# Performance work log

Measured on AMD Instinct MI355X. Metric: run time of the kernel, lower is better.

Reference implementation:

```python
import jax, jax.numpy as jnp
import numpy as np

B, N, D, F, L, R = 16, 1024, 256, 128, 2, 2


def setup_inputs() -> dict:
    key = jax.random.key(0)
    ks = jax.random.split(key, 12)
    s = 0.05
    return {
        "node_embed": jax.random.normal(ks[0], (B, N, D), jnp.float32),
        "input_x": jax.random.normal(ks[1], (B, F), jnp.float32),
        "adj": jax.random.randint(ks[2], (R, B, N, N), 0, 2, jnp.int32),
        "WQi_w": jax.random.normal(ks[3], (L, F, F), jnp.float32) * s,
        "WQi_b": jnp.zeros((L, F), jnp.float32),
        "WQ_w": jax.random.normal(ks[4], (L, D + F, D), jnp.float32) * s,
        "WQ_b": jnp.zeros((L, D), jnp.float32),
        "WK_w": jax.random.normal(ks[5], (L, R, D + F, D), jnp.float32) * s,
        "WK_b": jnp.zeros((L, R, D), jnp.float32),
        "WV_w": jax.random.normal(ks[6], (L, R, D + F, D), jnp.float32) * s,
        "WV_b": jnp.zeros((L, R, D), jnp.float32),
        "WF_w": jax.random.normal(ks[7], (L, R * D, D), jnp.float32) * s,
        "WF_b": jnp.zeros((L, D), jnp.float32),
        "ln_g": jnp.ones((L, D), jnp.float32),
        "ln_b": jnp.zeros((L, D), jnp.float32),
    }


def _layer_norm(x, g, b, eps=1e-5):
    mu = jnp.mean(x, axis=-1, keepdims=True)
    var = jnp.var(x, axis=-1, keepdims=True)
    return (x - mu) * jax.lax.rsqrt(var + eps) * g + b


def reference(node_embed, input_x, adj, WQi_w, WQi_b, WQ_w, WQ_b,
              WK_w, WK_b, WV_w, WV_b, WF_w, WF_b, ln_g, ln_b):
    scale = 1.0 / (D ** 0.5)
    h = node_embed
    for l in range(L):
        # input feature projection, broadcast over nodes
        x1 = input_x @ WQi_w[l] + WQi_b[l]              # (B, F)
        x1 = jnp.broadcast_to(x1[:, None, :], (h.shape[0], h.shape[1], F))
        qc = jnp.concatenate([h, x1], axis=-1)          # (B, N, D+F)
        q = qc @ WQ_w[l] + WQ_b[l]                      # (B, N, D)
        outs = []
        for r in range(R):
            k = qc @ WK_w[l, r] + WK_b[l, r]            # (B, N, D)
            v = qc @ WV_w[l, r] + WV_b[l, r]            # (B, N, D)
            scores = jnp.einsum('bnd,bmd->bnm', q, k) * scale
            scores = jnp.where(adj[r] == 0, -1e9, scores)
            alpha = jax.nn.softmax(scores, axis=-1)
            outs.append(jnp.einsum('bnm,bmd->bnd', alpha, v))
        h_concat = jnp.concatenate(outs, axis=-1)       # (B, N, R*D)
        h_fused = jax.nn.relu(h_concat @ WF_w[l] + WF_b[l])
        h = _layer_norm(h + h_fused, ln_g[l], ln_b[l])
    return h
```

## Files before the change

kernel.cpp:

```cpp
#include <hip/hip_runtime.h>
#include <hip/hip_bf16.h>

#define BB 16
#define NN 1024
#define DD 256
#define FF_ 128
#define LL 2
#define RR 2
#define DF 384
#define MM (BB*NN)
#define NPROJ 1280
#define PK 768

typedef __attribute__((ext_vector_type(8))) short s16x8;
typedef __attribute__((ext_vector_type(4))) float f32x4;
typedef __attribute__((ext_vector_type(16))) float f32x16;
typedef __attribute__((ext_vector_type(2))) unsigned int u32x2;
typedef __attribute__((ext_vector_type(4))) unsigned int u32x4;
typedef __attribute__((ext_vector_type(4))) unsigned short us16x4;

__device__ __forceinline__ unsigned short f2bf(float f){
  unsigned u = __builtin_bit_cast(unsigned, f);
  u += 0x7fff + ((u >> 16) & 1);
  return (unsigned short)(u >> 16);
}

__device__ __forceinline__ void gload16(const void* g, void* l){
  __builtin_amdgcn_global_load_lds(
      (const __attribute__((address_space(1))) unsigned int*)g,
      (__attribute__((address_space(3))) unsigned int*)l, 16, 0, 0);
}

#define MFMA16(a,b,c) __builtin_amdgcn_mfma_f32_16x16x32_bf16((a),(b),(c),0,0,0)
#define MFMA32(a,b,c) __builtin_amdgcn_mfma_f32_32x32x16_bf16((a),(b),(c),0,0,0)

__global__ __launch_bounds__(256) void pack_adj(const int* __restrict__ adj,
                                                unsigned long long* __restrict__ bits){
  int w = threadIdx.x >> 6, lane = threadIdx.x & 63;
  size_t row = (size_t)blockIdx.x * 4 + w;
  const int* a = adj + row * NN;
  unsigned long long* brow = bits + row * 16;
  #pragma unroll
  for (int j = 0; j < 16; ++j){
    unsigned long long m = __ballot(a[j*64 + lane] != 0);
    if (lane == 0) brow[j] = m;
  }
}

#define PREP_WT   3840
#define PREP_WTF  1024
#define PREP_BALL 10
#define PREP_X1   16
#define PREP_H    2048
#define PREP_TOT  (PREP_WT+PREP_WTF+PREP_BALL+PREP_X1+PREP_H)

__global__ __launch_bounds__(256) void prep(
    const float* __restrict__ node, const float* __restrict__ inx,
    const float* __restrict__ WQi_w, const float* __restrict__ WQi_b,
    const float* __restrict__ WQ_w, const float* __restrict__ WK_w,
    const float* __restrict__ WV_w, const float* __restrict__ WQ_b,
    const float* __restrict__ WK_b, const float* __restrict__ WV_b,
    const float* __restrict__ WF_w,
    unsigned short* __restrict__ wtall, unsigned short* __restrict__ wtf,
    float* __restrict__ ball, unsigned short* __restrict__ x1bf,
    unsigned short* __restrict__ hbf){
  int bid = blockIdx.x, t = threadIdx.x;
  if (bid < PREP_WT){
    int o = bid*256 + t;
    int l = o / (NPROJ*DF); int oo = o - l*(NPROJ*DF);
    int n = oo / DF, k = oo - n*DF;
    const float* WQ = WQ_w + (size_t)l*DF*256;
    const float* WK = WK_w + (size_t)l*RR*DF*256;
    const float* WV = WV_w + (size_t)l*RR*DF*256;
    float v;
    if (n < 256)      v = WQ[(size_t)k*256 + n];
    else if (n < 768) v = WK[(size_t)((n-256)>>8)*(DF*256) + (size_t)k*256 + ((n-256)&255)];
    else              v = WV[(size_t)((n-768)>>8)*(DF*256) + (size_t)k*256 + ((n-768)&255)];
    wtall[o] = f2bf(v);
  } else if (bid < PREP_WT + PREP_WTF){
    int o = (bid - PREP_WT)*256 + t;
    int l = o >> 17; int oo = o & 131071;
    int n = oo >> 9, k = oo & 511;
    wtf[o] = f2bf(WF_w[(size_t)l*512*256 + (size_t)k*256 + n]);
  } else if (bid < PREP_WT + PREP_WTF + PREP_BALL){
    int o = (bid - PREP_WT - PREP_WTF)*256 + t;
    if (o < 2*NPROJ){
      int l = o / NPROJ, n = o - l*NPROJ;
      float v = (n < 256) ? WQ_b[l*256 + n]
              : (n < 768) ? WK_b[(size_t)l*512 + (n-256)]
                          : WV_b[(size_t)l*512 + (n-768)];
      ball[o] = v;
    }
  } else if (bid < PREP_WT + PREP_WTF + PREP_BALL + PREP_X1){
    int o = (bid - PREP_WT - PREP_WTF - PREP_BALL)*256 + t;
    int l = o >> 11, bj = o & 2047;
    int b = bj >> 7, j = bj & 127;
    const float* w = WQi_w + (size_t)l*FF_*FF_;
    float s = WQi_b[l*FF_ + j];
    for (int i = 0; i < FF_; ++i) s += inx[b*FF_ + i] * w[i*FF_ + j];
    x1bf[o] = f2bf(s);
  } else {
    int o = (bid - (PREP_TOT - PREP_H))*256 + t;
    const float4* src = (const float4*)node + (size_t)o*2;
    float4 a = src[0], c = src[1];
    uint4 pk;
    pk.x = (unsigned)f2bf(a.x) | ((unsigned)f2bf(a.y) << 16);
    pk.y = (unsigned)f2bf(a.z) | ((unsigned)f2bf(a.w) << 16);
    pk.z = (unsigned)f2bf(c.x) | ((unsigned)f2bf(c.y) << 16);
    pk.w = (unsigned)f2bf(c.z) | ((unsigned)f2bf(c.w) << 16);
    *(uint4*)(hbf + (size_t)o*8) = pk;
  }
}

__global__ __launch_bounds__(256) void gemm_big(const unsigned short* __restrict__ hbf,
    const unsigned short* __restrict__ x1l, const unsigned short* __restrict__ Wt,
    const float* __restrict__ bias, unsigned short* __restrict__ POUT,
    unsigned short* __restrict__ vtall){
  __shared__ unsigned short As[2][128*32];
  __shared__ unsigned short Bs[2][128*32];
  int t = threadIdx.x, lane = t & 63, w = t >> 6;
  int wr = w >> 1, wc = w & 1, l15 = lane & 15, lhi = lane >> 4;
  int bm = blockIdx.x, bn = blockIdx.y, bb = bm >> 3;
  f32x4 acc[4][4];
  #pragma unroll
  for (int m = 0; m < 4; ++m)
    #pragma unroll
    for (int n = 0; n < 4; ++n) acc[m][n] = (f32x4){0.f,0.f,0.f,0.f};

  auto STAGE = [&](int bi, int kk){
    #pragma unroll
    for (int i = 0; i < 2; ++i){
      int base = w*2048 + i*1024;
      int off = base + lane*16;
      int row = off >> 6, cb = off & 63;
      const char* asrc = (kk < 8)
        ? (const char*)hbf + ((size_t)(bm*128 + row)*256 + kk*32)*2 + cb
        : (const char*)x1l + ((size_t)bb*128 + (kk-8)*32)*2 + cb;
      gload16(asrc, (char*)As[bi] + base);
      gload16((const char*)Wt + ((size_t)(bn*128 + row)*DF + kk*32)*2 + cb,
              (char*)Bs[bi] + base);
    }
  };

  STAGE(0, 0);
  __syncthreads();
  for (int kk = 0; kk < 12; ++kk){
    int cur = kk & 1;
    if (kk + 1 < 12) STAGE(cur ^ 1, kk + 1);
    s16x8 af[4], bfr[4];
    #pragma unroll
    for (int m = 0; m < 4; ++m) af[m]  = *(const s16x8*)&As[cur][(wr*64 + m*16 + l15)*32 + lhi*8];
    #pragma unroll
    for (int n = 0; n < 4; ++n) bfr[n] = *(const s16x8*)&Bs[cur][(wc*64 + n*16 + l15)*32 + lhi*8];
    __builtin_amdgcn_s_setprio(1);
    #pragma unroll
    for (int m = 0; m < 4; ++m)
      #pragma unroll
      for (int n = 0; n < 4; ++n)
        acc[m][n] = MFMA16(af[m], bfr[n], acc[m][n]);
    __builtin_amdgcn_s_setprio(0);
    __syncthreads();
  }

  if (bn < 6){
    #pragma unroll
    for (int n = 0; n < 4; ++n){
      int gn = bn*128 + wc*64 + n*16 + l15;
      float bv = bias[gn];
      #pragma unroll
      for (int m = 0; m < 4; ++m){
        int gm = bm*128 + wr*64 + m*16 + lhi*4;
        #pragma unroll
        for (int i = 0; i < 4; ++i)
          POUT[(size_t)(gm + i)*PK + gn] = f2bf(acc[m][n][i] + bv);
      }
    }
  } else {
    #pragma unroll
    for (int n = 0; n < 4; ++n){
      int gn = bn*128 + wc*64 + n*16 + l15;
      float bv = bias[gn];
      int rv = gn - 768;
      int r = rv >> 8, d = rv & 255;
      #pragma unroll
      for (int m = 0; m < 4; ++m){
        int mb = (bm & 7)*128 + wr*64 + m*16 + lhi*4;
        us16x4 pk;
        #pragma unroll
        for (int i = 0; i < 4; ++i) pk[i] = f2bf(acc[m][n][i] + bv);
        *(us16x4*)(vtall + ((size_t)((r*16 + bb)*256 + d))*NN + mb) = pk;
      }
    }
  }
}

__global__ __launch_bounds__(512, 2) void attn6(const unsigned short* __restrict__ P,
    const unsigned short* __restrict__ VT, const unsigned long long* __restrict__ bits,
    unsigned short* __restrict__ hc){
  __shared__ char smem[135168];

  int t = threadIdx.x, lane = t & 63, w = t >> 6;
  int h = lane >> 5, l31 = lane & 31;
  int hh = w >> 2, qs = w & 3;
  int F = blockIdx.x;
  int xcd = F & 7, j = F >> 3;
  int qt = j & 7;
  int gidx = xcd*4 + (j >> 3);
  int b = gidx & 15, r = gidx >> 4;
  const float C = 0.09016844f;

  size_t kcol = 256 + (size_t)r*256;
  const unsigned short* Vb = VT + ((size_t)(r*16 + b))*256*NN;

  int qrow = qt*128 + qs*32 + l31;

  s16x8 qf[16];
  {
    const unsigned short* qp = P + ((size_t)(b*NN + qrow))*PK + h*8;
    #pragma unroll
    for (int d_ = 0; d_ < 16; ++d_) qf[d_] = *(const s16x8*)(qp + d_*16);
  }

  f32x16 acc[8];
  #pragma unroll
  for (int dt = 0; dt < 8; ++dt)
    #pragma unroll
    for (int i = 0; i < 16; ++i) acc[dt][i] = 0.f;
  float mrow = -3e38f, lrow = 0.f;
  const unsigned long long* bitp = bits + ((size_t)(r*BB + b)*NN + qrow)*16;

  for (int it = 0; it < 8; ++it){
    __builtin_amdgcn_s_barrier();
    #pragma unroll
    for (int i = 0; i < 8; ++i){
      int o = i*8192 + w*1024 + lane*16;
      int hhs = o >> 15, local = o & 32767;
      int row = local >> 9, cb = local & 511;
      int scb = cb ^ ((row & 7) << 4);
      gload16((const char*)P + ((size_t)(b*NN + hhs*512 + it*64 + row)*PK + kcol)*2 + scb,
              smem + o);
    }
    #pragma unroll
    for (int i = 0; i < 8; ++i){
      int o = i*8192 + w*1024 + lane*16;
      int hhs = o >> 15, local = o & 32767;
      int vrow = local >> 7, cb = local & 127;
      int scb = cb ^ ((vrow & 7) << 4);
      gload16((const char*)Vb + ((size_t)vrow*NN + hhs*512 + it*64)*2 + scb,
              smem + 65536 + o);
    }
    unsigned long long mwv = bitp[hh*8 + it];
    asm volatile("s_waitcnt vmcnt(0)" ::: "memory");
    __builtin_amdgcn_s_barrier();
    __builtin_amdgcn_sched_barrier(0);

    const char* Kcur = smem + hh*32768;
    const char* Vcur = smem + 65536 + hh*32768;

    #pragma unroll
    for (int s = 0; s < 2; ++s){
      f32x16 st;
      #pragma unroll
      for (int i = 0; i < 16; ++i) st[i] = 0.f;
      int krow = s*32 + l31;
      int swzk = (krow & 7) << 4;
      const char* kbase = Kcur + krow*512;
      #pragma unroll
      for (int d_ = 0; d_ < 16; ++d_){
        s16x8 kf = *(const s16x8*)(kbase + ((d_*32 + h*16) ^ swzk));
        st = MFMA32(kf, qf[d_], st);
      }

      unsigned mw = (unsigned)(mwv >> (s*32));
      float tm = -3e38f;
      #pragma unroll
      for (int rr = 0; rr < 16; ++rr){
        int kb = (rr & 3) + 8*(rr >> 2) + 4*h;
        float sv = st[rr] * C;
        sv = ((mw >> kb) & 1u) ? sv : -1.443e9f;
        st[rr] = sv;
        tm = fmaxf(tm, sv);
      }
      tm = fmaxf(tm, __shfl_xor(tm, 32));
      if (tm > mrow + 10.f){
        float f = exp2f(mrow - tm);
        mrow = tm;
        lrow *= f;
        #pragma unroll
        for (int dt = 0; dt < 8; ++dt)
          #pragma unroll
          for (int i = 0; i < 16; ++i) acc[dt][i] *= f;
      }
      float rs = 0.f;
      #pragma unroll
      for (int rr = 0; rr < 16; ++rr){
        float e = exp2f(st[rr] - mrow);
        st[rr] = e;
        rs += e;
      }
      rs += __shfl_xor(rs, 32);
      lrow += rs;

      unsigned pk[8];
      #pragma unroll
      for (int p = 0; p < 8; ++p){
        unsigned rpk;
        float lo = st[p*2], hi = st[p*2+1];
        asm("v_cvt_pk_bf16_f32 %0, %1, %2" : "=v"(rpk) : "v"(lo), "v"(hi));
        pk[p] = rpk;
      }
      unsigned sA = h ? pk[0] : pk[2], sB = h ? pk[1] : pk[3];
      unsigned sC = h ? pk[4] : pk[6], sD = h ? pk[5] : pk[7];
      unsigned rxA = (unsigned)__shfl_xor((int)sA, 32);
      unsigned rxB = (unsigned)__shfl_xor((int)sB, 32);
      unsigned rxC = (unsigned)__shfl_xor((int)sC, 32);
      unsigned rxD = (unsigned)__shfl_xor((int)sD, 32);
      u32x4 pv0, pv1;
      pv0[0] = h ? rxA : pk[0]; pv0[1] = h ? rxB : pk[1];
      pv0[2] = h ? pk[2] : rxA; pv0[3] = h ? pk[3] : rxB;
      pv1[0] = h ? rxC : pk[4]; pv1[1] = h ? rxD : pk[5];
      pv1[2] = h ? pk[6] : rxC; pv1[3] = h ? pk[7] : rxD;
      s16x8 pa0 = __builtin_bit_cast(s16x8, pv0);
      s16x8 pa1 = __builtin_bit_cast(s16x8, pv1);

      #pragma unroll
      for (int dt = 0; dt < 8; ++dt){
        int vrow = dt*32 + l31;
        int swzv = (vrow & 7) << 4;
        const char* vbase = Vcur + vrow*128;
        s16x8 vf0 = *(const s16x8*)(vbase + (((2*s)*32 + h*16) ^ swzv));
        acc[dt] = MFMA32(vf0, pa0, acc[dt]);
        s16x8 vf1 = *(const s16x8*)(vbase + (((2*s+1)*32 + h*16) ^ swzv));
        acc[dt] = MFMA32(vf1, pa1, acc[dt]);
      }
    }
  }

  __builtin_amdgcn_s_barrier();
  if (hh){
    char* reg = smem + qs*33792 + lane*528;
    #pragma unroll
    for (int dt = 0; dt < 8; ++dt)
      #pragma unroll
      for (int g = 0; g < 4; ++g){
        f32x4 v;
        v[0] = acc[dt][g*4+0]; v[1] = acc[dt][g*4+1];
        v[2] = acc[dt][g*4+2]; v[3] = acc[dt][g*4+3];
        *(f32x4*)(reg + (dt*4+g)*16) = v;
      }
    *(float*)(reg + 512) = mrow;
    *(float*)(reg + 516) = lrow;
  }
  __builtin_amdgcn_s_barrier();
  if (!hh){
    const char* reg = smem + qs*33792 + lane*528;
    float m2 = *(const float*)(reg + 512);
    float l2 = *(const float*)(reg + 516);
    float m = fmaxf(mrow, m2);
    float w1 = exp2f(mrow - m), w2 = exp2f(m2 - m);
    float inv = 1.f / (lrow*w1 + l2*w2);
    float f1 = w1*inv, f2 = w2*inv;
    unsigned short* hrow = hc + ((size_t)(b*NN + qrow))*(RR*DD) + r*DD;
    #pragma unroll
    for (int dt = 0; dt < 8; ++dt){
      #pragma unroll
      for (int g = 0; g < 4; ++g){
        f32x4 a2 = *(const f32x4*)(reg + (dt*4+g)*16);
        float a0 = acc[dt][g*4+0]*f1 + a2[0]*f2;
        float a1 = acc[dt][g*4+1]*f1 + a2[1]*f2;
        float a2v = acc[dt][g*4+2]*f1 + a2[2]*f2;
        float a3 = acc[dt][g*4+3]*f1 + a2[3]*f2;
        unsigned r0, r1;
        asm("v_cvt_pk_bf16_f32 %0, %1, %2" : "=v"(r0) : "v"(a0), "v"(a1));
        asm("v_cvt_pk_bf16_f32 %0, %1, %2" : "=v"(r1) : "v"(a2v), "v"(a3));
        int d = dt*32 + 8*g + 4*h;
        u32x2 pv; pv[0] = r0; pv[1] = r1;
        *(u32x2*)(hrow + d) = pv;
      }
    }
  }
}

__global__ __launch_bounds__(256) void gemm_ff(const unsigned short* __restrict__ A,
    const unsigned short* __restrict__ Wt, const float* __restrict__ bias,
    float* __restrict__ out){
  __shared__ unsigned short As[2][128*32];
  __shared__ unsigned short Bs[2][128*32];
  int t = threadIdx.x, lane = t & 63, w = t >> 6;
  int wr = w >> 1, wc = w & 1, l15 = lane & 15, lhi = lane >> 4;
  int bm = blockIdx.x, bn = blockIdx.y;
  f32x4 acc[4][4];
  #pragma unroll
  for (int m = 0; m < 4; ++m)
    #pragma unroll
    for (int n = 0; n < 4; ++n) acc[m][n] = (f32x4){0.f,0.f,0.f,0.f};

  auto STAGE = [&](int bi, int kk){
    #pragma unroll
    for (int i = 0; i < 2; ++i){
      int base = w*2048 + i*1024;
      int off = base + lane*16;
      int row = off >> 6, cb = off & 63;
      gload16((const char*)A  + ((size_t)(bm*128 + row)*512 + kk*32)*2 + cb,
              (char*)As[bi] + base);
      gload16((const char*)Wt + ((size_t)(bn*128 + row)*512 + kk*32)*2 + cb,
              (char*)Bs[bi] + base);
    }
  };

  STAGE(0, 0);
  __syncthreads();
  for (int kk = 0; kk < 16; ++kk){
    int cur = kk & 1;
    if (kk + 1 < 16) STAGE(cur ^ 1, kk + 1);
    s16x8 af[4], bfr[4];
    #pragma unroll
    for (int m = 0; m < 4; ++m) af[m]  = *(const s16x8*)&As[cur][(wr*64 + m*16 + l15)*32 + lhi*8];
    #pragma unroll
    for (int n = 0; n < 4; ++n) bfr[n] = *(const s16x8*)&Bs[cur][(wc*64 + n*16 + l15)*32 + lhi*8];
    __builtin_amdgcn_s_setprio(1);
    #pragma unroll
    for (int m = 0; m < 4; ++m)
      #pragma unroll
      for (int n = 0; n < 4; ++n)
        acc[m][n] = MFMA16(af[m], bfr[n], acc[m][n]);
    __builtin_amdgcn_s_setprio(0);
    __syncthreads();
  }

  #pragma unroll
  for (int n = 0; n < 4; ++n){
    int gn = bn*128 + wc*64 + n*16 + l15;
    float bv = bias[gn];
    #pragma unroll
    for (int m = 0; m < 4; ++m){
      int gm = bm*128 + wr*64 + m*16 + lhi*4;
      #pragma unroll
      for (int i = 0; i < 4; ++i)
        out[(size_t)(gm + i)*DD + gn] = acc[m][n][i] + bv;
    }
  }
}

template<int WRITEH>
__global__ __launch_bounds__(256) void ln_res2(const float* __restrict__ ff,
    const float* __restrict__ hin, const float* __restrict__ g,
    const float* __restrict__ bv, float* __restrict__ hout,
    unsigned short* __restrict__ hbf){
  int w = threadIdx.x >> 6, lane = threadIdx.x & 63;
  size_t row = (size_t)blockIdx.x * 4 + w;
  f32x4 fv = *(const f32x4*)(ff  + row*DD + lane*4);
  f32x4 hv = *(const f32x4*)(hin + row*DD + lane*4);
  float x[4], s = 0.f, ss = 0.f;
  #pragma unroll
  for (int j = 0; j < 4; ++j){ x[j] = fmaxf(fv[j], 0.f) + hv[j]; s += x[j]; ss += x[j]*x[j]; }
  #pragma unroll
  for (int xm = 1; xm < 64; xm <<= 1){ s += __shfl_xor(s, xm); ss += __shfl_xor(ss, xm); }
  float mu = s * (1.f/256.f);
  float var = ss * (1.f/256.f) - mu*mu;
  float rstd = rsqrtf(var + 1e-5f);
  f32x4 o;
  #pragma unroll
  for (int j = 0; j < 4; ++j){ int c = lane*4 + j; o[j] = (x[j]-mu)*rstd*g[c] + bv[c]; }
  *(f32x4*)(hout + row*DD + lane*4) = o;
  if (WRITEH){
    uint2 pv;
    pv.x = (unsigned)f2bf(o[0]) | ((unsigned)f2bf(o[1]) << 16);
    pv.y = (unsigned)f2bf(o[2]) | ((unsigned)f2bf(o[3]) << 16);
    *(uint2*)(hbf + row*DD + lane*4) = pv;
  }
}

extern "C" void kernel_launch(void* const* d_in, const int* in_sizes, int n_in,
                              void* d_out, int out_size, void* d_ws, size_t ws_size,
                              hipStream_t stream){
  (void)in_sizes; (void)n_in; (void)out_size; (void)ws_size;
  const float* node  = (const float*)d_in[0];
  const float* inx   = (const float*)d_in[1];
  const int*   adj   = (const int*)d_in[2];
  const float* WQi_w = (const float*)d_in[3];
  const float* WQi_b = (const float*)d_in[4];
  const float* WQ_w  = (const float*)d_in[5];
  const float* WQ_b  = (const float*)d_in[6];
  const float* WK_w  = (const float*)d_in[7];
  const float* WK_b  = (const float*)d_in[8];
  const float* WV_w  = (const float*)d_in[9];
  const float* WV_b  = (const float*)d_in[10];
  const float* WF_w  = (const float*)d_in[11];
  const float* WF_b  = (const float*)d_in[12];
  const float* ln_g  = (const float*)d_in[13];
  const float* ln_b  = (const float*)d_in[14];
  float* hout = (float*)d_out;

  char* wsp = (char*)d_ws;
  auto alloc = [&](size_t n){ char* p = wsp; wsp += (n + 255) & ~(size_t)255; return p; };
  unsigned long long* bits = (unsigned long long*)alloc((size_t)RR*BB*NN*16*8);
  unsigned short* wtall = (unsigned short*)alloc((size_t)2*NPROJ*DF*2);
  unsigned short* wtf   = (unsigned short*)alloc((size_t)2*DD*512*2);
  float*          ball  = (float*)alloc((size_t)2*NPROJ*4);
  unsigned short* x1bf  = (unsigned short*)alloc((size_t)2*BB*FF_*2);
  unsigned short* hbf   = (unsigned short*)alloc((size_t)MM*DD*2);
  unsigned short* POUT  = (unsigned short*)alloc((size_t)MM*PK*2);
  unsigned short* vtall = (unsigned short*)alloc((size_t)RR*BB*DD*NN*2);
  unsigned short* hc    = (unsigned short*)alloc((size_t)MM*512*2);
  float*          ffo   = (float*)alloc((size_t)MM*DD*4);

  pack_adj<<<RR*BB*NN/4, 256, 0, stream>>>(adj, bits);
  prep<<<PREP_TOT, 256, 0, stream>>>(node, inx, WQi_w, WQi_b, WQ_w, WK_w, WV_w,
                                     WQ_b, WK_b, WV_b, WF_w,
                                     wtall, wtf, ball, x1bf, hbf);

  for (int l = 0; l < LL; ++l){
    gemm_big<<<dim3(128,10), 256, 0, stream>>>(hbf, x1bf + (size_t)l*BB*FF_,
        wtall + (size_t)l*NPROJ*DF, ball + (size_t)l*NPROJ, POUT, vtall);

    attn6<<<256, 512, 0, stream>>>(POUT, vtall, bits, hc);

    gemm_ff<<<dim3(128,2), 256, 0, stream>>>(hc, wtf + (size_t)l*DD*512, WF_b + l*DD, ffo);

    if (l == 0) ln_res2<1><<<MM/4, 256, 0, stream>>>(ffo, node, ln_g, ln_b, hout, hbf);
    else        ln_res2<0><<<MM/4, 256, 0, stream>>>(ffo, (const float*)hout,
                                                     ln_g + DD, ln_b + DD, hout, nullptr);
  }
}
```

Before: 360.3 us.

## Double-buffer K/V tiles in attention kernel and coalesce output via LDS staging

The attention kernel now splits the key loop into 16 smaller steps of 32 keys per half and double-buffers K and V tiles in shared memory. The next tile's global loads are issued before computing on the current one, with a partial vmcnt wait, so memory latency overlaps the MFMA and softmax work instead of stalling on every iteration. The epilogue stages the bf16 output in swizzled LDS and writes it out as full 16-byte rows for coalesced stores. This adds more barriers per key and extra synchronisation in the epilogue, and the per-iteration mask load now happens inside the compute path.

After: 337.5 us. 6.3% less time.

```diff
diff --git a/kernel.cpp b/kernel.cpp
--- a/kernel.cpp
+++ b/kernel.cpp
@@ -194,7 +194,7 @@
   }
 }
 
-__global__ __launch_bounds__(512, 2) void attn6(const unsigned short* __restrict__ P,
+__global__ __launch_bounds__(512, 2) void attn7(const unsigned short* __restrict__ P,
     const unsigned short* __restrict__ VT, const unsigned long long* __restrict__ bits,
     unsigned short* __restrict__ hc){
   __shared__ char smem[135168];
@@ -211,7 +211,6 @@
 
   size_t kcol = 256 + (size_t)r*256;
   const unsigned short* Vb = VT + ((size_t)(r*16 + b))*256*NN;
-
   int qrow = qt*128 + qs*32 + l31;
 
   s16x8 qf[16];
@@ -220,6 +219,7 @@
     #pragma unroll
     for (int d_ = 0; d_ < 16; ++d_) qf[d_] = *(const s16x8*)(qp + d_*16);
   }
+  asm volatile("s_waitcnt vmcnt(0)" ::: "memory");
 
   f32x16 acc[8];
   #pragma unroll
@@ -229,114 +229,121 @@
   float mrow = -3e38f, lrow = 0.f;
   const unsigned long long* bitp = bits + ((size_t)(r*BB + b)*NN + qrow)*16;
 
-  for (int it = 0; it < 8; ++it){
-    __builtin_amdgcn_s_barrier();
-    #pragma unroll
-    for (int i = 0; i < 8; ++i){
-      int o = i*8192 + w*1024 + lane*16;
-      int hhs = o >> 15, local = o & 32767;
-      int row = local >> 9, cb = local & 511;
-      int scb = cb ^ ((row & 7) << 4);
-      gload16((const char*)P + ((size_t)(b*NN + hhs*512 + it*64 + row)*PK + kcol)*2 + scb,
-              smem + o);
-    }
-    #pragma unroll
-    for (int i = 0; i < 8; ++i){
-      int o = i*8192 + w*1024 + lane*16;
-      int hhs = o >> 15, local = o & 32767;
-      int vrow = local >> 7, cb = local & 127;
-      int scb = cb ^ ((vrow & 7) << 4);
-      gload16((const char*)Vb + ((size_t)vrow*NN + hhs*512 + it*64)*2 + scb,
-              smem + 65536 + o);
-    }
-    unsigned long long mwv = bitp[hh*8 + it];
-    asm volatile("s_waitcnt vmcnt(0)" ::: "memory");
+  auto STAGE = [&](int buf, int it){
+    char* base = smem + buf*65536;
+    #pragma unroll
+    for (int i = 0; i < 4; ++i){
+      int o = i*8192 + t*16;
+      int kr = o >> 9, cb = o & 511;
+      int lcb = cb ^ ((kr & 7) << 4);
+      int gk = (kr >> 5)*512 + it*32 + (kr & 31);
+      gload16((const char*)P + ((size_t)(b*NN + gk)*PK + kcol)*2 + lcb, base + o);
+    }
+    #pragma unroll
+    for (int i = 0; i < 4; ++i){
+      int o = i*8192 + t*16;
+      int vr = o >> 7, cb = o & 127;
+      int lcb = cb ^ ((vr & 7) << 4);
+      gload16((const char*)Vb + ((size_t)vr*NN + (lcb >> 6)*512 + it*32)*2 + (lcb & 63),
+              base + 32768 + o);
+    }
+  };
+
+  STAGE(0, 0);
+
+  for (int it = 0; it < 16; ++it){
+    int cur = it & 1;
+    if (it + 1 < 16){
+      STAGE(cur ^ 1, it + 1);
+      asm volatile("s_waitcnt vmcnt(8)" ::: "memory");
+    } else {
+      asm volatile("s_waitcnt vmcnt(0)" ::: "memory");
+    }
     __builtin_amdgcn_s_barrier();
     __builtin_amdgcn_sched_barrier(0);
 
-    const char* Kcur = smem + hh*32768;
-    const char* Vcur = smem + 65536 + hh*32768;
-
-    #pragma unroll
-    for (int s = 0; s < 2; ++s){
-      f32x16 st;
-      #pragma unroll
-      for (int i = 0; i < 16; ++i) st[i] = 0.f;
-      int krow = s*32 + l31;
-      int swzk = (krow & 7) << 4;
-      const char* kbase = Kcur + krow*512;
-      #pragma unroll
-      for (int d_ = 0; d_ < 16; ++d_){
-        s16x8 kf = *(const s16x8*)(kbase + ((d_*32 + h*16) ^ swzk));
-        st = MFMA32(kf, qf[d_], st);
-      }
-
-      unsigned mw = (unsigned)(mwv >> (s*32));
-      float tm = -3e38f;
-      #pragma unroll
-      for (int rr = 0; rr < 16; ++rr){
-        int kb = (rr & 3) + 8*(rr >> 2) + 4*h;
-        float sv = st[rr] * C;
-        sv = ((mw >> kb) & 1u) ? sv : -1.443e9f;
-        st[rr] = sv;
-        tm = fmaxf(tm, sv);
-      }
-      tm = fmaxf(tm, __shfl_xor(tm, 32));
-      if (tm > mrow + 10.f){
-        float f = exp2f(mrow - tm);
-        mrow = tm;
-        lrow *= f;
+    const char* Kc = smem + cur*65536;
+    const char* Vc = smem + cur*65536 + 32768;
+
+    f32x16 st;
+    #pragma unroll
+    for (int i = 0; i < 16; ++i) st[i] = 0.f;
+    int krow = hh*32 + l31;
+    int swzk = (krow & 7) << 4;
+    const char* kbase = Kc + krow*512;
+    #pragma unroll
+    for (int d_ = 0; d_ < 16; ++d_){
+      s16x8 kf = *(const s16x8*)(kbase + ((d_*32 + h*16) ^ swzk));
+      st = MFMA32(kf, qf[d_], st);
+    }
+
+    unsigned mw = (unsigned)(bitp[hh*8 + (it >> 1)] >> ((it & 1)*32));
+    float tm = -3e38f;
+    #pragma unroll
+    for (int rr = 0; rr < 16; ++rr){
+      int kb = (rr & 3) + 8*(rr >> 2) + 4*h;
+      float sv = st[rr] * C;
+      sv = ((mw >> kb) & 1u) ? sv : -1.443e9f;
+      st[rr] = sv;
+      tm = fmaxf(tm, sv);
+    }
+    tm = fmaxf(tm, __shfl_xor(tm, 32));
+    if (tm > mrow + 10.f){
+      float f = exp2f(mrow - tm);
+      mrow = tm;
+      lrow *= f;
+      #pragma unroll
+      for (int dt = 0; dt < 8; ++dt)
         #pragma unroll
-        for (int dt = 0; dt < 8; ++dt)
-          #pragma unroll
-          for (int i = 0; i < 16; ++i) acc[dt][i] *= f;
-      }
-      float rs = 0.f;
-      #pragma unroll
-      for (int rr = 0; rr < 16; ++rr){
-        float e = exp2f(st[rr] - mrow);
-        st[rr] = e;
-        rs += e;
-      }
-      rs += __shfl_xor(rs, 32);
-      lrow += rs;
-
-      unsigned pk[8];
-      #pragma unroll
-      for (int p = 0; p < 8; ++p){
-        unsigned rpk;
-        float lo = st[p*2], hi = st[p*2+1];
-        asm("v_cvt_pk_bf16_f32 %0, %1, %2" : "=v"(rpk) : "v"(lo), "v"(hi));
-        pk[p] = rpk;
-      }
-      unsigned sA = h ? pk[0] : pk[2], sB = h ? pk[1] : pk[3];
-      unsigned sC = h ? pk[4] : pk[6], sD = h ? pk[5] : pk[7];
-      unsigned rxA = (unsigned)__shfl_xor((int)sA, 32);
-      unsigned rxB = (unsigned)__shfl_xor((int)sB, 32);
-      unsigned rxC = (unsigned)__shfl_xor((int)sC, 32);
-      unsigned rxD = (unsigned)__shfl_xor((int)sD, 32);
-      u32x4 pv0, pv1;
-      pv0[0] = h ? rxA : pk[0]; pv0[1] = h ? rxB : pk[1];
-      pv0[2] = h ? pk[2] : rxA; pv0[3] = h ? pk[3] : rxB;
-      pv1[0] = h ? rxC : pk[4]; pv1[1] = h ? rxD : pk[5];
-      pv1[2] = h ? pk[6] : rxC; pv1[3] = h ? pk[7] : rxD;
-      s16x8 pa0 = __builtin_bit_cast(s16x8, pv0);
-      s16x8 pa1 = __builtin_bit_cast(s16x8, pv1);
-
-      #pragma unroll
-      for (int dt = 0; dt < 8; ++dt){
-        int vrow = dt*32 + l31;
-        int swzv = (vrow & 7) << 4;
-        const char* vbase = Vcur + vrow*128;
-        s16x8 vf0 = *(const s16x8*)(vbase + (((2*s)*32 + h*16) ^ swzv));
-        acc[dt] = MFMA32(vf0, pa0, acc[dt]);
-        s16x8 vf1 = *(const s16x8*)(vbase + (((2*s+1)*32 + h*16) ^ swzv));
-        acc[dt] = MFMA32(vf1, pa1, acc[dt]);
-      }
-    }
-  }
-
-  __builtin_amdgcn_s_barrier();
+        for (int i = 0; i < 16; ++i) acc[dt][i] *= f;
+    }
+    float rs = 0.f;
+    #pragma unroll
+    for (int rr = 0; rr < 16; ++rr){
+      float e = exp2f(st[rr] - mrow);
+      st[rr] = e;
+      rs += e;
+    }
+    rs += __shfl_xor(rs, 32);
+    lrow += rs;
+
+    unsigned pk[8];
+    #pragma unroll
+    for (int p = 0; p < 8; ++p){
+      unsigned rpk;
+      float lo = st[p*2], hi = st[p*2+1];
+      asm("v_cvt_pk_bf16_f32 %0, %1, %2" : "=v"(rpk) : "v"(lo), "v"(hi));
+      pk[p] = rpk;
+    }
+    unsigned sA = h ? pk[0] : pk[2], sB = h ? pk[1] : pk[3];
+    unsigned sC = h ? pk[4] : pk[6], sD = h ? pk[5] : pk[7];
+    unsigned rxA = (unsigned)__shfl_xor((int)sA, 32);
+    unsigned rxB = (unsigned)__shfl_xor((int)sB, 32);
+    unsigned rxC = (unsigned)__shfl_xor((int)sC, 32);
+    unsigned rxD = (unsigned)__shfl_xor((int)sD, 32);
+    u32x4 pv0, pv1;
+    pv0[0] = h ? rxA : pk[0]; pv0[1] = h ? rxB : pk[1];
+    pv0[2] = h ? pk[2] : rxA; pv0[3] = h ? pk[3] : rxB;
+    pv1[0] = h ? rxC : pk[4]; pv1[1] = h ? rxD : pk[5];
+    pv1[2] = h ? pk[6] : rxC; pv1[3] = h ? pk[7] : rxD;
+    s16x8 pa0 = __builtin_bit_cast(s16x8, pv0);
+    s16x8 pa1 = __builtin_bit_cast(s16x8, pv1);
+
+    #pragma unroll
+    for (int dt = 0; dt < 8; ++dt){
+      int vr = dt*32 + l31;
+      int swzv = (vr & 7) << 4;
+      const char* vbase = Vc + vr*128;
+      s16x8 vf0 = *(const s16x8*)(vbase + ((hh*64 + h*16) ^ swzv));
+      acc[dt] = MFMA32(vf0, pa0, acc[dt]);
+      s16x8 vf1 = *(const s16x8*)(vbase + ((hh*64 + 32 + h*16) ^ swzv));
+      acc[dt] = MFMA32(vf1, pa1, acc[dt]);
+    }
+
+    __builtin_amdgcn_s_barrier();
+  }
+
+  __syncthreads();
   if (hh){
     char* reg = smem + qs*33792 + lane*528;
     #pragma unroll
@@ -351,7 +358,7 @@
     *(float*)(reg + 512) = mrow;
     *(float*)(reg + 516) = lrow;
   }
-  __builtin_amdgcn_s_barrier();
+  __syncthreads();
   if (!hh){
     const char* reg = smem + qs*33792 + lane*528;
     float m2 = *(const float*)(reg + 512);
@@ -360,24 +367,45 @@
     float w1 = exp2f(mrow - m), w2 = exp2f(m2 - m);
     float inv = 1.f / (lrow*w1 + l2*w2);
     float f1 = w1*inv, f2 = w2*inv;
-    unsigned short* hrow = hc + ((size_t)(b*NN + qrow))*(RR*DD) + r*DD;
-    #pragma unroll
-    for (int dt = 0; dt < 8; ++dt){
+    #pragma unroll
+    for (int dt = 0; dt < 8; ++dt)
       #pragma unroll
       for (int g = 0; g < 4; ++g){
         f32x4 a2 = *(const f32x4*)(reg + (dt*4+g)*16);
-        float a0 = acc[dt][g*4+0]*f1 + a2[0]*f2;
-        float a1 = acc[dt][g*4+1]*f1 + a2[1]*f2;
-        float a2v = acc[dt][g*4+2]*f1 + a2[2]*f2;
-        float a3 = acc[dt][g*4+3]*f1 + a2[3]*f2;
+        acc[dt][g*4+0] = acc[dt][g*4+0]*f1 + a2[0]*f2;
+        acc[dt][g*4+1] = acc[dt][g*4+1]*f1 + a2[1]*f2;
+        acc[dt][g*4+2] = acc[dt][g*4+2]*f1 + a2[2]*f2;
+        acc[dt][g*4+3] = acc[dt][g*4+3]*f1 + a2[3]*f2;
+      }
+  }
+  __syncthreads();
+  if (!hh){
+    unsigned short* Ob = (unsigned short*)smem;
+    int qloc = qs*32 + l31;
+    #pragma unroll
+    for (int dt = 0; dt < 8; ++dt)
+      #pragma unroll
+      for (int g = 0; g < 4; ++g){
+        float a0 = acc[dt][g*4+0], a1 = acc[dt][g*4+1];
+        float a2v = acc[dt][g*4+2], a3 = acc[dt][g*4+3];
         unsigned r0, r1;
         asm("v_cvt_pk_bf16_f32 %0, %1, %2" : "=v"(r0) : "v"(a0), "v"(a1));
         asm("v_cvt_pk_bf16_f32 %0, %1, %2" : "=v"(r1) : "v"(a2v), "v"(a3));
         int d = dt*32 + 8*g + 4*h;
+        int byteoff = qloc*512 + ((d*2) ^ ((qloc & 7) << 4));
         u32x2 pv; pv[0] = r0; pv[1] = r1;
-        *(u32x2*)(hrow + d) = pv;
+        *(u32x2*)((char*)Ob + byteoff) = pv;
       }
-    }
+  }
+  __syncthreads();
+  #pragma unroll
+  for (int it = 0; it < 8; ++it){
+    int off = (it*512 + t) * 16;
+    int row = off >> 9, cb = off & 511;
+    int scb = cb ^ ((row & 7) << 4);
+    u32x4 v = *(const u32x4*)(smem + row*512 + scb);
+    int q = qt*128 + row;
+    *(u32x4*)((char*)hc + (((size_t)(b*NN + q))*512 + r*256 + (cb >> 1))*2) = v;
   }
 }
 
@@ -514,7 +542,7 @@
     gemm_big<<<dim3(128,10), 256, 0, stream>>>(hbf, x1bf + (size_t)l*BB*FF_,
         wtall + (size_t)l*NPROJ*DF, ball + (size_t)l*NPROJ, POUT, vtall);
 
-    attn6<<<256, 512, 0, stream>>>(POUT, vtall, bits, hc);
+    attn7<<<256, 512, 0, stream>>>(POUT, vtall, bits, hc);
 
     gemm_ff<<<dim3(128,2), 256, 0, stream>>>(hc, wtf + (size_t)l*DD*512, WF_b + l*DD, ffo);
 
```
